# Performance work log

Measured on AMD Instinct MI355X. Metric: run time of the kernel, lower is better.

## Reference

```python
import jax, jax.numpy as jnp
import numpy as np

N_QUBITS = 12
N_LAYERS = 4
INPUT_DIM = 64
N_CLASSES = 4
BATCH = 2048


def _ry_mat(theta):
    # RY(t) = [[cos t/2, -sin t/2], [sin t/2, cos t/2]], returned as [..., 2, 2] complex64
    c = jnp.cos(theta / 2).astype(jnp.complex64)
    s = jnp.sin(theta / 2).astype(jnp.complex64)
    return jnp.stack([jnp.stack([c, -s], -1), jnp.stack([s, c], -1)], -2)


def _rz_mat(theta):
    # RZ(t) = diag(e^{-i t/2}, e^{+i t/2}), [..., 2, 2] complex64
    ph = jnp.exp((-0.5j) * theta).astype(jnp.complex64)
    z = jnp.zeros_like(ph)
    return jnp.stack([jnp.stack([ph, z], -1), jnp.stack([z, jnp.conj(ph)], -1)], -2)


def _apply_1q_batched(state, gate, wire):
    # state: [B] + [2]*n, gate: [B, 2, 2] (per-sample gate, e.g. angle encoding)
    ax = wire + 1
    st = jnp.moveaxis(state, ax, -1)
    st = jnp.einsum('b...i,bji->b...j', st, gate)
    return jnp.moveaxis(st, -1, ax)


def _apply_1q_shared(state, gate, wire):
    # state: [B] + [2]*n, gate: [2, 2] (shared trainable gate)
    ax = wire + 1
    st = jnp.moveaxis(state, ax, -1)
    st = jnp.einsum('...i,ji->...j', st, gate)
    return jnp.moveaxis(st, -1, ax)


def _cnot(state, control, target):
    ca, ta = control + 1, target + 1
    s0 = jax.lax.index_in_dim(state, 0, ca, keepdims=True)
    s1 = jax.lax.index_in_dim(state, 1, ca, keepdims=True)
    s1 = jnp.flip(s1, ta)  # X on target when control = 1
    return jnp.concatenate([s0, s1], axis=ca)


def _simulate(angles, qw):
    # angles: [B, n] encoding angles; qw: [L, n, 2] variational params
    B, n = angles.shape
    state = jnp.zeros((B,) + (2,) * n, jnp.complex64)
    state = state.at[(slice(None),) + (0,) * n].set(1.0 + 0.0j)
    enc = _ry_mat(angles)  # [B, n, 2, 2]
    for q in range(n):
        state = _apply_1q_batched(state, enc[:, q], q)
    for l in range(qw.shape[0]):
        ryg = _ry_mat(qw[l, :, 0])  # [n, 2, 2]
        rzg = _rz_mat(qw[l, :, 1])  # [n, 2, 2]
        for q in range(n):
            state = _apply_1q_shared(state, ryg[q], q)
            state = _apply_1q_shared(state, rzg[q], q)
        for q in range(n - 1):
            state = _cnot(state, q, q + 1)
        if n > 1:
            state = _cnot(state, n - 1, 0)
    p = state.real ** 2 + state.imag ** 2  # probabilities, [B] + [2]*n
    zs = []
    for q in range(n):
        m = jnp.moveaxis(p, q + 1, 1).reshape(B, 2, -1).sum(-1)  # [B, 2]
        zs.append(m[:, 0] - m[:, 1])
    return jnp.stack(zs, -1)  # [B, n] PauliZ expectations


def setup_inputs() -> dict:
    key = jax.random.key(0)
    ks = jax.random.split(key, 4)
    x = jax.random.normal(ks[0], (BATCH, INPUT_DIM), dtype=jnp.float32)
    W_in = 0.1 * jax.random.normal(ks[1], (N_QUBITS, INPUT_DIM), dtype=jnp.float32)
    b_in = jnp.zeros((N_QUBITS,), dtype=jnp.float32)
    qw = 0.01 * jax.random.normal(ks[2], (N_LAYERS, N_QUBITS, 2), dtype=jnp.float32)
    W_out = 0.1 * jax.random.normal(ks[3], (N_CLASSES, N_QUBITS), dtype=jnp.float32)
    b_out = jnp.zeros((N_CLASSES,), dtype=jnp.float32)
    return {"compressed_features": x, "W_in": W_in, "b_in": b_in, "qw": qw,
            "W_out": W_out, "b_out": b_out}


def reference(compressed_features, W_in, b_in, qw, W_out, b_out):
    angles = jnp.tanh(compressed_features @ W_in.T + b_in) * jnp.float32(np.pi)  # [B, n]
    zfeat = _simulate(angles, qw)  # [B, n]
    return zfeat @ W_out.T + b_out  # [B, n_classes]
```

## Files before the change

### kernel.cpp

```cpp
#include <hip/hip_runtime.h>
#include <math.h>

#define NQ    12
#define NST   4096
#define NL    4
#define NBATCH 2048
#define DIM   64
#define NCLS  4
#define TPB   512
#define APT   8

typedef float v2f __attribute__((ext_vector_type(2)));

constexpr unsigned Pm(unsigned j) { return j ^ (j >> 1) ^ ((j & 1u) * 0xC00u); }

constexpr unsigned Lm(unsigned j) {
    return (j & ~0x1Fu) | ((j ^ (j >> 3)) & 0xFu) | ((((j >> 4) ^ (j >> 8)) & 1u) << 4);
}

__device__ __forceinline__ unsigned beta_of(int lane, int wv) {
    return ((unsigned)(lane >> 4) & 1u)       | (((unsigned)wv & 1u) << 1)
         | (((unsigned)(wv >> 1) & 1u) << 2)  | (((unsigned)(wv >> 2) & 1u) << 3)
         | (((unsigned)(lane >> 2) & 1u) << 4)| (((unsigned)lane & 1u) << 5)
         | (((unsigned)(lane >> 5) & 1u) << 6)| (((unsigned)(lane >> 1) & 1u) << 7)
         | (((unsigned)(lane >> 3) & 1u) << 8);
}

__device__ __forceinline__ v2f cmul(v2f x, v2f y) {
    v2f r; r.x = x.x*y.x - x.y*y.y; r.y = x.x*y.y + x.y*y.x; return r;
}

template<int XB>
__device__ __forceinline__ float lx(float v) {
    int i = __float_as_int(v);
    if constexpr (XB == 1) {
        return __int_as_float(__builtin_amdgcn_update_dpp(i, i, 0xB1, 0xF, 0xF, true));
    } else if constexpr (XB == 2) {
        return __int_as_float(__builtin_amdgcn_update_dpp(i, i, 0x4E, 0xF, 0xF, true));
    } else {
        return __int_as_float(__builtin_amdgcn_update_dpp(i, i, 0x128, 0xF, 0xF, true));
    }
}

template<int P>
__device__ __forceinline__ void intra_g(v2f (&a)[APT], float c, float s) {
    #pragma unroll
    for (int k = 0; k < APT; ++k) {
        if (!(k & (1 << P))) {
            const int k1 = k | (1 << P);
            v2f x0 = a[k], x1 = a[k1];
            a[k]  = c*x0 - s*x1;
            a[k1] = s*x0 + c*x1;
        }
    }
}

template<int XB>
__device__ __forceinline__ void lane_g(v2f (&a)[APT], float c, float s, int lane) {
    const float Br = (lane & XB) ? s : -s;
    #pragma unroll
    for (int k = 0; k < APT; ++k) {
        v2f o; o.x = lx<XB>(a[k].x); o.y = lx<XB>(a[k].y);
        a[k] = c*a[k] + Br*o;
    }
}

__device__ __forceinline__ void gates_A(v2f (&a)[APT], const float* __restrict__ cs, int lane) {
    intra_g<0>(a, cs[11*2], cs[11*2+1]);
    intra_g<1>(a, cs[10*2], cs[10*2+1]);
    intra_g<2>(a, cs[ 9*2], cs[ 9*2+1]);
    lane_g<1>(a, cs[8*2], cs[8*2+1], lane);
    lane_g<2>(a, cs[7*2], cs[7*2+1], lane);
    lane_g<8>(a, cs[5*2], cs[5*2+1], lane);
}
__device__ __forceinline__ void gates_B(v2f (&a)[APT], const float* __restrict__ cs, int lane) {
    intra_g<0>(a, cs[2*2], cs[2*2+1]);
    intra_g<1>(a, cs[1*2], cs[1*2+1]);
    intra_g<2>(a, cs[0*2], cs[0*2+1]);
    lane_g<1>(a, cs[6*2], cs[6*2+1], lane);
    lane_g<2>(a, cs[4*2], cs[4*2+1], lane);
    lane_g<8>(a, cs[3*2], cs[3*2+1], lane);
}

__global__ void vqc_setup(const float* __restrict__ qw, float* __restrict__ gp) {
    const int t = threadIdx.x;
    const int lane = t & 63, wv = t >> 6;
    if (t < 36) {
        int l = t / 12 + 1, q = t % 12;
        float th = qw[(l*NQ + q)*2];
        float cc, ss; sincosf(0.5f*th, &ss, &cc);
        gp[((l-1)*NQ + q)*2 + 0] = cc;
        gp[((l-1)*NQ + q)*2 + 1] = ss;
    }
    if (t >= 64 && t < 80) {
        int i = t - 64, l = i/8 + 1, k = i%8;
        float ang = 0.f;
        if (k & 1) ang += qw[(l*NQ + 2)*2 + 1];
        if (k & 2) ang += qw[(l*NQ + 1)*2 + 1];
        if (k & 4) ang += qw[(l*NQ + 0)*2 + 1];
        float s_, c_; sincosf(ang, &s_, &c_);
        gp[72 + (l-1)*16 + k*2 + 0] = c_;
        gp[72 + (l-1)*16 + k*2 + 1] = s_;
    }
    const unsigned be = beta_of(lane, wv);
    #pragma unroll
    for (int l = 1; l <= 2; ++l) {
        float ang = 0.f;
        #pragma unroll
        for (int b = 0; b <= 8; ++b)
            if ((be >> b) & 1) ang += qw[(l*NQ + (11 - b))*2 + 1];
        float s_, c_; sincosf(ang, &s_, &c_);
        gp[104 + (l-1)*1024 + t*2 + 0] = c_;
        gp[104 + (l-1)*1024 + t*2 + 1] = s_;
    }
}

__global__ __launch_bounds__(TPB, 4) void vqc_kernel(
    const float* __restrict__ x,
    const float* __restrict__ Win,
    const float* __restrict__ bin,
    const float* __restrict__ qw,
    const float* __restrict__ Wout,
    const float* __restrict__ bout,
    const float* __restrict__ gp,
    float* __restrict__ out)
{
    __shared__ __align__(16) v2f buf[NST];
    __shared__ float xs[DIM];
    __shared__ float g0c[NQ], g0r[NQ], g0i[NQ];
    __shared__ float zred[8][9];
    __shared__ float zfin[NQ];

    const int tid  = threadIdx.x;
    const int lane = tid & 63;
    const int wv   = tid >> 6;
    const int b    = blockIdx.x;

    const unsigned al  = (unsigned)tid << 3;
    const unsigned be  = beta_of(lane, wv);
    const unsigned LA1 = Lm(al),      LB1 = Lm(be);
    const unsigned LA2 = Lm(Pm(al)),  LB2 = Lm(Pm(be));
    const unsigned LA3 = Lm(Pm(Pm(al))), LB3 = Lm(Pm(Pm(be)));

    if (tid < DIM) xs[tid] = x[b*DIM + tid];
    __syncthreads();

    if (tid < 192) {
        const int q = tid >> 4, r = tid & 15;
        float acc = xs[r] * Win[q*DIM + r]
                  + xs[r+16] * Win[q*DIM + r + 16]
                  + xs[r+32] * Win[q*DIM + r + 32]
                  + xs[r+48] * Win[q*DIM + r + 48];
        acc += __shfl_xor(acc, 8, 16);
        acc += __shfl_xor(acc, 4, 16);
        acc += __shfl_xor(acc, 2, 16);
        acc += __shfl_xor(acc, 1, 16);
        if (r == 0) {
            acc += bin[q];
            float ang = tanhf(acc) * 3.14159265358979323846f;
            float th  = ang + qw[(0*NQ + q)*2 + 0];
            float ph  = qw[(0*NQ + q)*2 + 1];
            float cc, ss; sincosf(0.5f*th, &ss, &cc);
            float pcv, psv; sincosf(ph, &psv, &pcv);
            g0c[q] = cc; g0r[q] = ss*pcv; g0i[q] = ss*psv;
        }
    }
    __syncthreads();

    v2f a[APT];

    {
        const unsigned nb = Pm(al);
        v2f thrP = (v2f){1.f, 0.f};
        #pragma unroll
        for (int bb = 3; bb <= 9; ++bb) {
            const int q = 11 - bb;
            const bool bit = (nb >> bb) & 1u;
            v2f f; f.x = bit ? g0r[q] : g0c[q]; f.y = bit ? g0i[q] : 0.f;
            thrP = cmul(thrP, f);
        }
        const bool n10 = (nb >> 10) & 1u, n11 = (nb >> 11) & 1u;
        v2f f1b; f1b.x = n10 ? g0r[1] : g0c[1]; f1b.y = n10 ? g0i[1] : 0.f;
        v2f f1x; f1x.x = n10 ? g0c[1] : g0r[1]; f1x.y = n10 ? 0.f : g0i[1];
        v2f f0b; f0b.x = n11 ? g0r[0] : g0c[0]; f0b.y = n11 ? g0i[0] : 0.f;
        v2f f0x; f0x.x = n11 ? g0c[0] : g0r[0]; f0x.y = n11 ? 0.f : g0i[0];
        v2f C0 = cmul(thrP, cmul(f1b, f0b));
        v2f C1 = cmul(thrP, cmul(f1x, f0x));
        const bool n0 = nb & 1u, n1 = (nb >> 1) & 1u, n2 = (nb >> 2) & 1u;
        v2f fa; fa.x = n0 ? g0r[11] : g0c[11]; fa.y = n0 ? g0i[11] : 0.f;
        v2f fb; fb.x = n0 ? g0c[11] : g0r[11]; fb.y = n0 ? 0.f : g0i[11];
        v2f E0 = cmul(C0, fa), E1 = cmul(C0, fb);
        v2f F0 = cmul(C1, fb), F1 = cmul(C1, fa);
        v2f u10; u10.x = n1 ? g0r[10] : g0c[10]; u10.y = n1 ? g0i[10] : 0.f;
        v2f w10; w10.x = n1 ? g0c[10] : g0r[10]; w10.y = n1 ? 0.f : g0i[10];
        v2f u9;  u9.x  = n2 ? g0r[9]  : g0c[9];  u9.y  = n2 ? g0i[9]  : 0.f;
        v2f w9;  w9.x  = n2 ? g0c[9]  : g0r[9];  w9.y  = n2 ? 0.f : g0i[9];
        v2f G0 = cmul(u10, u9), G1 = cmul(w10, u9), G2 = cmul(w10, w9), G3 = cmul(u10, w9);
        a[0] = cmul(E0, G0); a[1] = cmul(F0, G0);
        a[2] = cmul(E1, G1); a[3] = cmul(F1, G1);
        a[4] = cmul(E0, G2); a[5] = cmul(F0, G2);
        a[6] = cmul(E1, G3); a[7] = cmul(F1, G3);
    }

    const float* cs1 = gp;
    const float* cs2 = gp + 24;
    const float* cs3 = gp + 48;
    const v2f thrD1 = *(const v2f*)(gp + 104 + tid*2);
    const v2f thrD2 = *(const v2f*)(gp + 104 + 1024 + tid*2);

    gates_A(a, cs1, lane);
    {
        float4* f4 = (float4*)buf;
        const bool a0 = LA1 & 1u;
        #pragma unroll
        for (int ke = 0; ke < APT; ke += 2) {
            v2f lo = a0 ? a[ke+1] : a[ke];
            v2f hi = a0 ? a[ke]   : a[ke+1];
            f4[(LA1 ^ (unsigned)ke) >> 1] = make_float4(lo.x, lo.y, hi.x, hi.y);
        }
    }
    __syncthreads();
    #pragma unroll
    for (int k = 0; k < APT; ++k) a[k] = buf[LB1 ^ ((unsigned)k << 9)];
    gates_B(a, cs1, lane);
    #pragma unroll
    for (int k = 0; k < APT; ++k) {
        v2f kd = *(const v2f*)(gp + 72 + k*2);
        a[k] = cmul(a[k], cmul(thrD1, kd));
    }
    #pragma unroll
    for (int k = 0; k < APT; ++k) buf[LB1 ^ ((unsigned)k << 9)] = a[k];
    __syncthreads();

    #pragma unroll
    for (int k = 0; k < APT; ++k) a[k] = buf[LA2 ^ Lm(Pm((unsigned)k))];
    gates_A(a, cs2, lane);
    #pragma unroll
    for (int k = 0; k < APT; ++k) buf[LA2 ^ Lm(Pm((unsigned)k))] = a[k];
    __syncthreads();
    #pragma unroll
    for (int k = 0; k < APT; ++k) a[k] = buf[LB2 ^ Lm(Pm((unsigned)k << 9))];
    gates_B(a, cs2, lane);
    #pragma unroll
    for (int k = 0; k < APT; ++k) {
        v2f kd = *(const v2f*)(gp + 72 + 16 + k*2);
        a[k] = cmul(a[k], cmul(thrD2, kd));
    }
    #pragma unroll
    for (int k = 0; k < APT; ++k) buf[LB2 ^ Lm(Pm((unsigned)k << 9))] = a[k];
    __syncthreads();

    #pragma unroll
    for (int k = 0; k < APT; ++k) a[k] = buf[LA3 ^ Lm(Pm(Pm((unsigned)k)))];
    gates_A(a, cs3, lane);
    #pragma unroll
    for (int k = 0; k < APT; ++k) buf[LA3 ^ Lm(Pm(Pm((unsigned)k)))] = a[k];
    __syncthreads();
    #pragma unroll
    for (int k = 0; k < APT; ++k) a[k] = buf[LB3 ^ Lm(Pm(Pm((unsigned)k << 9)))];
    gates_B(a, cs3, lane);

    {
        float p[APT];
        #pragma unroll
        for (int k = 0; k < APT; ++k) p[k] = a[k].x*a[k].x + a[k].y*a[k].y;
        float A = (p[0]-p[1]) - (p[2]-p[3]), B = (p[4]-p[5]) - (p[6]-p[7]);
        float C = (p[0]+p[1]) - (p[2]+p[3]), D = (p[4]+p[5]) - (p[6]+p[7]);
        float w7 = A - B;
        float w3 = A + B;
        float w6 = C - D;
        #pragma unroll
        for (int t = 0; t < 6; ++t) {
            float o7 = __shfl_xor(w7, 1 << t, 64);
            float o6 = __shfl_xor(w6, 1 << t, 64);
            float o3 = __shfl_xor(w3, 1 << t, 64);
            const bool hi = (lane >> t) & 1;
            w7 = hi ? (o7 - w7) : (w7 + o7);
            w6 = hi ? (o6 - w6) : (w6 + o6);
            w3 = hi ? (o3 - w3) : (w3 + o3);
        }
        if      (lane == 63) { zred[wv][0] = w7; zred[wv][8] = w3; }
        else if (lane == 47) { zred[wv][1] = w7; }
        else if (lane == 43) { zred[wv][2] = w7; }
        else if (lane == 42) { zred[wv][3] = w7; }
        else if (lane == 10) { zred[wv][4] = w7; }
        else if (lane ==  8) { zred[wv][5] = w7; }
        else if (lane ==  0) { zred[wv][6] = w7; zred[wv][7] = w6; }
    }
    __syncthreads();
    if (tid < NQ) {
        const int p = 11 - tid;
        const int slot = (p == 0) ? 0 : (p <= 4) ? 1 : (p - 3);
        const int wm = (p <= 1 || p == 11) ? 7 : (p == 2) ? 6 : (p == 3) ? 4 : 0;
        float acc = 0.f;
        #pragma unroll
        for (int W = 0; W < 8; ++W) {
            float v = zred[W][slot];
            acc += (__popc(W & wm) & 1) ? -v : v;
        }
        zfin[tid] = acc;
    }
    __syncthreads();

    if (tid < NCLS) {
        float acc = bout[tid];
        #pragma unroll
        for (int q = 0; q < NQ; ++q) acc += zfin[q] * Wout[tid*NQ + q];
        out[b*NCLS + tid] = acc;
    }
}

extern "C" void kernel_launch(void* const* d_in, const int* in_sizes, int n_in,
                              void* d_out, int out_size, void* d_ws, size_t ws_size,
                              hipStream_t stream) {
    const float* x    = (const float*)d_in[0];
    const float* Win  = (const float*)d_in[1];
    const float* bin  = (const float*)d_in[2];
    const float* qw   = (const float*)d_in[3];
    const float* Wout = (const float*)d_in[4];
    const float* bout = (const float*)d_in[5];
    float* gp  = (float*)d_ws;
    float* out = (float*)d_out;
    hipLaunchKernelGGL(vqc_setup, dim3(1), dim3(TPB), 0, stream, qw, gp);
    hipLaunchKernelGGL(vqc_kernel, dim3(NBATCH), dim3(TPB), 0, stream,
                       x, Win, bin, qw, Wout, bout, gp, out);
}
```

Baseline: 53.37 us.

## Halve threads per block with 16 amplitudes per thread and new swizzle

Each block now uses 256 threads, and each thread holds 16 state amplitudes instead of 8. Four qubits are applied in registers per pass, with two via DPP lane exchanges, so the 8-way xor lane gate is dropped. The shared-memory swizzle, the phase tables and the final Z-reduction bit bookkeeping are all rewritten for this layout. Gate math uses packed v_pk_fma/v_pk_mul instructions, and the separate store loop after the diagonal phase is fused into the multiply. This removes one DPP gate type and halves wave count per block, but it raises register pressure and reduces parallelism per block.

```diff
diff --git a/kernel.cpp b/kernel.cpp
--- a/kernel.cpp
+++ b/kernel.cpp
@@ -3,115 +3,113 @@
 
 #define NQ    12
 #define NST   4096
-#define NL    4
 #define NBATCH 2048
 #define DIM   64
 #define NCLS  4
-#define TPB   512
-#define APT   8
+#define TPB   256
+#define APT   16
 
 typedef float v2f __attribute__((ext_vector_type(2)));
 
 constexpr unsigned Pm(unsigned j) { return j ^ (j >> 1) ^ ((j & 1u) * 0xC00u); }
-
-constexpr unsigned Lm(unsigned j) {
-    return (j & ~0x1Fu) | ((j ^ (j >> 3)) & 0xFu) | ((((j >> 4) ^ (j >> 8)) & 1u) << 4);
-}
-
-__device__ __forceinline__ unsigned beta_of(int lane, int wv) {
-    return ((unsigned)(lane >> 4) & 1u)       | (((unsigned)wv & 1u) << 1)
-         | (((unsigned)(wv >> 1) & 1u) << 2)  | (((unsigned)(wv >> 2) & 1u) << 3)
-         | (((unsigned)(lane >> 2) & 1u) << 4)| (((unsigned)lane & 1u) << 5)
-         | (((unsigned)(lane >> 5) & 1u) << 6)| (((unsigned)(lane >> 1) & 1u) << 7)
-         | (((unsigned)(lane >> 3) & 1u) << 8);
+constexpr unsigned Sm(unsigned j) { return j ^ ((j >> 4) & 0xFu); }
+
+__device__ __forceinline__ unsigned alphaA(unsigned t) { return t << 4; }
+__device__ __forceinline__ unsigned alphaB(unsigned t) {
+    unsigned lane = t & 63u, w = t >> 6;
+    return ((lane >> 2) & 0xFu) | (w << 4) | ((lane & 3u) << 6);
 }
 
 __device__ __forceinline__ v2f cmul(v2f x, v2f y) {
     v2f r; r.x = x.x*y.x - x.y*y.y; r.y = x.x*y.y + x.y*y.x; return r;
+}
+
+__device__ __forceinline__ v2f pk_mul(v2f a, v2f b) {
+    v2f d; asm("v_pk_mul_f32 %0, %1, %2" : "=v"(d) : "v"(a), "v"(b)); return d;
+}
+__device__ __forceinline__ v2f pk_fma(v2f a, v2f b, v2f c) {
+    v2f d; asm("v_pk_fma_f32 %0, %1, %2, %3" : "=v"(d) : "v"(a), "v"(b), "v"(c)); return d;
 }
 
 template<int XB>
 __device__ __forceinline__ float lx(float v) {
     int i = __float_as_int(v);
-    if constexpr (XB == 1) {
+    if constexpr (XB == 1)
         return __int_as_float(__builtin_amdgcn_update_dpp(i, i, 0xB1, 0xF, 0xF, true));
-    } else if constexpr (XB == 2) {
+    else
         return __int_as_float(__builtin_amdgcn_update_dpp(i, i, 0x4E, 0xF, 0xF, true));
-    } else {
-        return __int_as_float(__builtin_amdgcn_update_dpp(i, i, 0x128, 0xF, 0xF, true));
-    }
 }
 
 template<int P>
 __device__ __forceinline__ void intra_g(v2f (&a)[APT], float c, float s) {
+    const v2f cc = {c, c}, ss = {s, s}, ns = {-s, -s};
     #pragma unroll
     for (int k = 0; k < APT; ++k) {
         if (!(k & (1 << P))) {
             const int k1 = k | (1 << P);
             v2f x0 = a[k], x1 = a[k1];
-            a[k]  = c*x0 - s*x1;
-            a[k1] = s*x0 + c*x1;
+            a[k]  = pk_fma(ns, x1, pk_mul(cc, x0));
+            a[k1] = pk_fma(cc, x1, pk_mul(ss, x0));
         }
     }
 }
 
 template<int XB>
 __device__ __forceinline__ void lane_g(v2f (&a)[APT], float c, float s, int lane) {
-    const float Br = (lane & XB) ? s : -s;
+    const float br = (lane & XB) ? s : -s;
+    const v2f cc = {c, c}, bb = {br, br};
     #pragma unroll
     for (int k = 0; k < APT; ++k) {
         v2f o; o.x = lx<XB>(a[k].x); o.y = lx<XB>(a[k].y);
-        a[k] = c*a[k] + Br*o;
+        a[k] = pk_fma(bb, o, pk_mul(cc, a[k]));
     }
 }
 
 __device__ __forceinline__ void gates_A(v2f (&a)[APT], const float* __restrict__ cs, int lane) {
-    intra_g<0>(a, cs[11*2], cs[11*2+1]);
-    intra_g<1>(a, cs[10*2], cs[10*2+1]);
-    intra_g<2>(a, cs[ 9*2], cs[ 9*2+1]);
-    lane_g<1>(a, cs[8*2], cs[8*2+1], lane);
-    lane_g<2>(a, cs[7*2], cs[7*2+1], lane);
-    lane_g<8>(a, cs[5*2], cs[5*2+1], lane);
+    intra_g<0>(a, cs[22], cs[23]);
+    intra_g<1>(a, cs[20], cs[21]);
+    intra_g<2>(a, cs[18], cs[19]);
+    intra_g<3>(a, cs[16], cs[17]);
+    lane_g<1>(a, cs[14], cs[15], lane);
+    lane_g<2>(a, cs[12], cs[13], lane);
 }
 __device__ __forceinline__ void gates_B(v2f (&a)[APT], const float* __restrict__ cs, int lane) {
-    intra_g<0>(a, cs[2*2], cs[2*2+1]);
-    intra_g<1>(a, cs[1*2], cs[1*2+1]);
-    intra_g<2>(a, cs[0*2], cs[0*2+1]);
-    lane_g<1>(a, cs[6*2], cs[6*2+1], lane);
-    lane_g<2>(a, cs[4*2], cs[4*2+1], lane);
-    lane_g<8>(a, cs[3*2], cs[3*2+1], lane);
+    intra_g<0>(a, cs[6], cs[7]);
+    intra_g<1>(a, cs[4], cs[5]);
+    intra_g<2>(a, cs[2], cs[3]);
+    intra_g<3>(a, cs[0], cs[1]);
+    lane_g<1>(a, cs[10], cs[11], lane);
+    lane_g<2>(a, cs[8],  cs[9],  lane);
 }
 
 __global__ void vqc_setup(const float* __restrict__ qw, float* __restrict__ gp) {
     const int t = threadIdx.x;
-    const int lane = t & 63, wv = t >> 6;
     if (t < 36) {
         int l = t / 12 + 1, q = t % 12;
-        float th = qw[(l*NQ + q)*2];
-        float cc, ss; sincosf(0.5f*th, &ss, &cc);
-        gp[((l-1)*NQ + q)*2 + 0] = cc;
-        gp[((l-1)*NQ + q)*2 + 1] = ss;
-    }
-    if (t >= 64 && t < 80) {
-        int i = t - 64, l = i/8 + 1, k = i%8;
+        float cc, ss; sincosf(0.5f * qw[(l*NQ + q)*2], &ss, &cc);
+        gp[(l-1)*24 + q*2 + 0] = cc;
+        gp[(l-1)*24 + q*2 + 1] = ss;
+    }
+    if (t < 32) {
+        int l = t / 16 + 1, k = t % 16;
         float ang = 0.f;
-        if (k & 1) ang += qw[(l*NQ + 2)*2 + 1];
-        if (k & 2) ang += qw[(l*NQ + 1)*2 + 1];
-        if (k & 4) ang += qw[(l*NQ + 0)*2 + 1];
+        #pragma unroll
+        for (int i = 0; i < 4; ++i)
+            if ((k >> i) & 1) ang += qw[(l*NQ + (3 - i))*2 + 1];
         float s_, c_; sincosf(ang, &s_, &c_);
-        gp[72 + (l-1)*16 + k*2 + 0] = c_;
-        gp[72 + (l-1)*16 + k*2 + 1] = s_;
-    }
-    const unsigned be = beta_of(lane, wv);
+        gp[72 + (l-1)*32 + k*2 + 0] = c_;
+        gp[72 + (l-1)*32 + k*2 + 1] = s_;
+    }
+    const unsigned j = alphaB((unsigned)t);
     #pragma unroll
     for (int l = 1; l <= 2; ++l) {
         float ang = 0.f;
         #pragma unroll
-        for (int b = 0; b <= 8; ++b)
-            if ((be >> b) & 1) ang += qw[(l*NQ + (11 - b))*2 + 1];
+        for (int b = 0; b < 8; ++b)
+            if ((j >> b) & 1) ang += qw[(l*NQ + (11 - b))*2 + 1];
         float s_, c_; sincosf(ang, &s_, &c_);
-        gp[104 + (l-1)*1024 + t*2 + 0] = c_;
-        gp[104 + (l-1)*1024 + t*2 + 1] = s_;
+        gp[136 + (l-1)*512 + t*2 + 0] = c_;
+        gp[136 + (l-1)*512 + t*2 + 1] = s_;
     }
 }
 
@@ -128,7 +126,7 @@
     __shared__ __align__(16) v2f buf[NST];
     __shared__ float xs[DIM];
     __shared__ float g0c[NQ], g0r[NQ], g0i[NQ];
-    __shared__ float zred[8][9];
+    __shared__ float zred[4][10];
     __shared__ float zfin[NQ];
 
     const int tid  = threadIdx.x;
@@ -136,11 +134,10 @@
     const int wv   = tid >> 6;
     const int b    = blockIdx.x;
 
-    const unsigned al  = (unsigned)tid << 3;
-    const unsigned be  = beta_of(lane, wv);
-    const unsigned LA1 = Lm(al),      LB1 = Lm(be);
-    const unsigned LA2 = Lm(Pm(al)),  LB2 = Lm(Pm(be));
-    const unsigned LA3 = Lm(Pm(Pm(al))), LB3 = Lm(Pm(Pm(be)));
+    const unsigned aA = alphaA((unsigned)tid), aB = alphaB((unsigned)tid);
+    const unsigned A1 = Sm(aA),         B1 = Sm(aB);
+    const unsigned A2 = Sm(Pm(aA)),     B2 = Sm(Pm(aB));
+    const unsigned A3 = Sm(Pm(Pm(aA))), B3 = Sm(Pm(Pm(aB)));
 
     if (tid < DIM) xs[tid] = x[b*DIM + tid];
     __syncthreads();
@@ -170,132 +167,143 @@
     v2f a[APT];
 
     {
-        const unsigned nb = Pm(al);
+        const unsigned nb = Pm(aA);
         v2f thrP = (v2f){1.f, 0.f};
         #pragma unroll
-        for (int bb = 3; bb <= 9; ++bb) {
+        for (int bb = 4; bb <= 9; ++bb) {
             const int q = 11 - bb;
             const bool bit = (nb >> bb) & 1u;
             v2f f; f.x = bit ? g0r[q] : g0c[q]; f.y = bit ? g0i[q] : 0.f;
             thrP = cmul(thrP, f);
         }
         const bool n10 = (nb >> 10) & 1u, n11 = (nb >> 11) & 1u;
-        v2f f1b; f1b.x = n10 ? g0r[1] : g0c[1]; f1b.y = n10 ? g0i[1] : 0.f;
-        v2f f1x; f1x.x = n10 ? g0c[1] : g0r[1]; f1x.y = n10 ? 0.f : g0i[1];
-        v2f f0b; f0b.x = n11 ? g0r[0] : g0c[0]; f0b.y = n11 ? g0i[0] : 0.f;
-        v2f f0x; f0x.x = n11 ? g0c[0] : g0r[0]; f0x.y = n11 ? 0.f : g0i[0];
-        v2f C0 = cmul(thrP, cmul(f1b, f0b));
-        v2f C1 = cmul(thrP, cmul(f1x, f0x));
-        const bool n0 = nb & 1u, n1 = (nb >> 1) & 1u, n2 = (nb >> 2) & 1u;
-        v2f fa; fa.x = n0 ? g0r[11] : g0c[11]; fa.y = n0 ? g0i[11] : 0.f;
-        v2f fb; fb.x = n0 ? g0c[11] : g0r[11]; fb.y = n0 ? 0.f : g0i[11];
-        v2f E0 = cmul(C0, fa), E1 = cmul(C0, fb);
-        v2f F0 = cmul(C1, fb), F1 = cmul(C1, fa);
-        v2f u10; u10.x = n1 ? g0r[10] : g0c[10]; u10.y = n1 ? g0i[10] : 0.f;
-        v2f w10; w10.x = n1 ? g0c[10] : g0r[10]; w10.y = n1 ? 0.f : g0i[10];
-        v2f u9;  u9.x  = n2 ? g0r[9]  : g0c[9];  u9.y  = n2 ? g0i[9]  : 0.f;
-        v2f w9;  w9.x  = n2 ? g0c[9]  : g0r[9];  w9.y  = n2 ? 0.f : g0i[9];
-        v2f G0 = cmul(u10, u9), G1 = cmul(w10, u9), G2 = cmul(w10, w9), G3 = cmul(u10, w9);
-        a[0] = cmul(E0, G0); a[1] = cmul(F0, G0);
-        a[2] = cmul(E1, G1); a[3] = cmul(F1, G1);
-        a[4] = cmul(E0, G2); a[5] = cmul(F0, G2);
-        a[6] = cmul(E1, G3); a[7] = cmul(F1, G3);
-    }
-
-    const float* cs1 = gp;
-    const float* cs2 = gp + 24;
-    const float* cs3 = gp + 48;
-    const v2f thrD1 = *(const v2f*)(gp + 104 + tid*2);
-    const v2f thrD2 = *(const v2f*)(gp + 104 + 1024 + tid*2);
+        v2f h10a; h10a.x = n10 ? g0r[1] : g0c[1]; h10a.y = n10 ? g0i[1] : 0.f;
+        v2f h10b; h10b.x = n10 ? g0c[1] : g0r[1]; h10b.y = n10 ? 0.f : g0i[1];
+        v2f h11a; h11a.x = n11 ? g0r[0] : g0c[0]; h11a.y = n11 ? g0i[0] : 0.f;
+        v2f h11b; h11b.x = n11 ? g0c[0] : g0r[0]; h11b.y = n11 ? 0.f : g0i[0];
+        v2f TT0 = cmul(thrP, cmul(h10a, h11a));
+        v2f TT1 = cmul(thrP, cmul(h10b, h11b));
+        v2f u[4], w[4];
+        #pragma unroll
+        for (int bb = 0; bb < 4; ++bb) {
+            const int q = 11 - bb;
+            const bool bit = (nb >> bb) & 1u;
+            u[bb].x = bit ? g0r[q] : g0c[q]; u[bb].y = bit ? g0i[q] : 0.f;
+            w[bb].x = bit ? g0c[q] : g0r[q]; w[bb].y = bit ? 0.f : g0i[q];
+        }
+        v2f P01[4], P23[4];
+        #pragma unroll
+        for (int c = 0; c < 4; ++c) {
+            P01[c] = cmul((c & 1) ? w[0] : u[0], (c & 2) ? w[1] : u[1]);
+            P23[c] = cmul((c & 1) ? w[2] : u[2], (c & 2) ? w[3] : u[3]);
+        }
+        #pragma unroll
+        for (int k = 0; k < APT; ++k) {
+            const unsigned kp = (unsigned)k ^ ((unsigned)k >> 1);
+            v2f g = cmul(P01[kp & 3], P23[(kp >> 2) & 3]);
+            a[k] = cmul((k & 1) ? TT1 : TT0, g);
+        }
+    }
+
+    const float* cs1 = gp, *cs2 = gp + 24, *cs3 = gp + 48;
+    const v2f tD1 = *(const v2f*)(gp + 136 + tid*2);
+    const v2f tD2 = *(const v2f*)(gp + 136 + 512 + tid*2);
 
     gates_A(a, cs1, lane);
     {
         float4* f4 = (float4*)buf;
-        const bool a0 = LA1 & 1u;
+        const int a0 = (int)(A1 & 1u);
         #pragma unroll
         for (int ke = 0; ke < APT; ke += 2) {
             v2f lo = a0 ? a[ke+1] : a[ke];
             v2f hi = a0 ? a[ke]   : a[ke+1];
-            f4[(LA1 ^ (unsigned)ke) >> 1] = make_float4(lo.x, lo.y, hi.x, hi.y);
-        }
-    }
-    __syncthreads();
-    #pragma unroll
-    for (int k = 0; k < APT; ++k) a[k] = buf[LB1 ^ ((unsigned)k << 9)];
+            f4[(A1 ^ (unsigned)ke) >> 1] = make_float4(lo.x, lo.y, hi.x, hi.y);
+        }
+    }
+    __syncthreads();
+    #pragma unroll
+    for (int k = 0; k < APT; ++k) a[k] = buf[B1 ^ ((unsigned)k << 8)];
     gates_B(a, cs1, lane);
     #pragma unroll
     for (int k = 0; k < APT; ++k) {
         v2f kd = *(const v2f*)(gp + 72 + k*2);
-        a[k] = cmul(a[k], cmul(thrD1, kd));
-    }
-    #pragma unroll
-    for (int k = 0; k < APT; ++k) buf[LB1 ^ ((unsigned)k << 9)] = a[k];
-    __syncthreads();
-
-    #pragma unroll
-    for (int k = 0; k < APT; ++k) a[k] = buf[LA2 ^ Lm(Pm((unsigned)k))];
+        buf[B1 ^ ((unsigned)k << 8)] = cmul(cmul(a[k], tD1), kd);
+    }
+    __syncthreads();
+
+    #pragma unroll
+    for (int k = 0; k < APT; ++k) a[k] = buf[A2 ^ Sm(Pm((unsigned)k))];
     gates_A(a, cs2, lane);
     #pragma unroll
-    for (int k = 0; k < APT; ++k) buf[LA2 ^ Lm(Pm((unsigned)k))] = a[k];
-    __syncthreads();
-    #pragma unroll
-    for (int k = 0; k < APT; ++k) a[k] = buf[LB2 ^ Lm(Pm((unsigned)k << 9))];
+    for (int k = 0; k < APT; ++k) buf[A2 ^ Sm(Pm((unsigned)k))] = a[k];
+    __syncthreads();
+    #pragma unroll
+    for (int k = 0; k < APT; ++k) a[k] = buf[B2 ^ Sm(Pm((unsigned)k << 8))];
     gates_B(a, cs2, lane);
     #pragma unroll
     for (int k = 0; k < APT; ++k) {
-        v2f kd = *(const v2f*)(gp + 72 + 16 + k*2);
-        a[k] = cmul(a[k], cmul(thrD2, kd));
-    }
-    #pragma unroll
-    for (int k = 0; k < APT; ++k) buf[LB2 ^ Lm(Pm((unsigned)k << 9))] = a[k];
-    __syncthreads();
-
-    #pragma unroll
-    for (int k = 0; k < APT; ++k) a[k] = buf[LA3 ^ Lm(Pm(Pm((unsigned)k)))];
+        v2f kd = *(const v2f*)(gp + 72 + 32 + k*2);
+        buf[B2 ^ Sm(Pm((unsigned)k << 8))] = cmul(cmul(a[k], tD2), kd);
+    }
+    __syncthreads();
+
+    #pragma unroll
+    for (int k = 0; k < APT; ++k) a[k] = buf[A3 ^ Sm(Pm(Pm((unsigned)k)))];
     gates_A(a, cs3, lane);
     #pragma unroll
-    for (int k = 0; k < APT; ++k) buf[LA3 ^ Lm(Pm(Pm((unsigned)k)))] = a[k];
-    __syncthreads();
-    #pragma unroll
-    for (int k = 0; k < APT; ++k) a[k] = buf[LB3 ^ Lm(Pm(Pm((unsigned)k << 9)))];
+    for (int k = 0; k < APT; ++k) buf[A3 ^ Sm(Pm(Pm((unsigned)k)))] = a[k];
+    __syncthreads();
+    #pragma unroll
+    for (int k = 0; k < APT; ++k) a[k] = buf[B3 ^ Sm(Pm(Pm((unsigned)k << 8)))];
     gates_B(a, cs3, lane);
 
     {
         float p[APT];
         #pragma unroll
-        for (int k = 0; k < APT; ++k) p[k] = a[k].x*a[k].x + a[k].y*a[k].y;
-        float A = (p[0]-p[1]) - (p[2]-p[3]), B = (p[4]-p[5]) - (p[6]-p[7]);
-        float C = (p[0]+p[1]) - (p[2]+p[3]), D = (p[4]+p[5]) - (p[6]+p[7]);
-        float w7 = A - B;
-        float w3 = A + B;
-        float w6 = C - D;
+        for (int k = 0; k < APT; ++k) p[k] = fmaf(a[k].x, a[k].x, a[k].y*a[k].y);
+        float A_[8], Bm[8];
+        #pragma unroll
+        for (int j = 0; j < 8; ++j) { A_[j] = p[2*j] + p[2*j+1]; Bm[j] = p[2*j] - p[2*j+1]; }
+        float AA[4], AB[4], BB[4];
+        #pragma unroll
+        for (int i = 0; i < 4; ++i) {
+            AA[i] = A_[2*i] + A_[2*i+1];
+            AB[i] = A_[2*i] - A_[2*i+1];
+            BB[i] = Bm[2*i] - Bm[2*i+1];
+        }
+        float WF = BB[0] - BB[1] - BB[2] + BB[3];
+        float W7 = BB[0] - BB[1] + BB[2] - BB[3];
+        float WE = AB[0] - AB[1] - AB[2] + AB[3];
+        float WC = AA[0] - AA[1] - AA[2] + AA[3];
         #pragma unroll
         for (int t = 0; t < 6; ++t) {
-            float o7 = __shfl_xor(w7, 1 << t, 64);
-            float o6 = __shfl_xor(w6, 1 << t, 64);
-            float o3 = __shfl_xor(w3, 1 << t, 64);
+            float oF = __shfl_xor(WF, 1 << t, 64);
+            float o7 = __shfl_xor(W7, 1 << t, 64);
+            float oE = __shfl_xor(WE, 1 << t, 64);
+            float oC = __shfl_xor(WC, 1 << t, 64);
             const bool hi = (lane >> t) & 1;
-            w7 = hi ? (o7 - w7) : (w7 + o7);
-            w6 = hi ? (o6 - w6) : (w6 + o6);
-            w3 = hi ? (o3 - w3) : (w3 + o3);
-        }
-        if      (lane == 63) { zred[wv][0] = w7; zred[wv][8] = w3; }
-        else if (lane == 47) { zred[wv][1] = w7; }
-        else if (lane == 43) { zred[wv][2] = w7; }
-        else if (lane == 42) { zred[wv][3] = w7; }
-        else if (lane == 10) { zred[wv][4] = w7; }
-        else if (lane ==  8) { zred[wv][5] = w7; }
-        else if (lane ==  0) { zred[wv][6] = w7; zred[wv][7] = w6; }
+            WF = hi ? (oF - WF) : (WF + oF);
+            W7 = hi ? (o7 - W7) : (W7 + o7);
+            WE = hi ? (oE - WE) : (WE + oE);
+            WC = hi ? (oC - WC) : (WC + oC);
+        }
+        if      (lane == 63) { zred[wv][0] = WF; zred[wv][9] = W7; }
+        else if (lane == 59) { zred[wv][1] = WF; }
+        else if (lane == 51) { zred[wv][2] = WF; }
+        else if (lane == 35) { zred[wv][3] = WF; }
+        else if (lane ==  3) { zred[wv][4] = WF; }
+        else if (lane ==  2) { zred[wv][5] = WF; }
+        else if (lane ==  0) { zred[wv][6] = WF; zred[wv][7] = WE; zred[wv][8] = WC; }
     }
     __syncthreads();
     if (tid < NQ) {
-        const int p = 11 - tid;
-        const int slot = (p == 0) ? 0 : (p <= 4) ? 1 : (p - 3);
-        const int wm = (p <= 1 || p == 11) ? 7 : (p == 2) ? 6 : (p == 3) ? 4 : 0;
+        const int slotT[12] = {9,8,7,6,5,4,4,4,3,2,1,0};
+        const int wmT[12]   = {3,0,0,0,0,0,2,3,3,3,3,3};
+        const int sl = slotT[tid], wm = wmT[tid];
         float acc = 0.f;
         #pragma unroll
-        for (int W = 0; W < 8; ++W) {
-            float v = zred[W][slot];
+        for (int W = 0; W < 4; ++W) {
+            float v = zred[W][sl];
             acc += (__popc(W & wm) & 1) ? -v : v;
         }
         zfin[tid] = acc;
```

Measured after the change: 51.45 us. -3.6%, faster.

## Swap LDS swizzles for per-phase XOR maps and use packed FMA gates

Applied to the files above, without the earlier changes.

Replaces the single Lm shared-memory swizzle with separate per-phase XOR maps (T1m/T2m/T4m), so the read and write addresses of a phase can differ. This needs an extra barrier before each write-back. The single-qubit rotations now use inline-asm v_pk_mul/v_pk_fma on complex pairs to halve VALU instruction count. Launch bounds rise to 8 waves per EU, which may increase register pressure or spilling. The aim is fewer LDS bank conflicts and fewer ALU ops, at the cost of extra synchronisation.

```diff
diff --git a/kernel.cpp b/kernel.cpp
--- a/kernel.cpp
+++ b/kernel.cpp
@@ -3,7 +3,6 @@
 
 #define NQ    12
 #define NST   4096
-#define NL    4
 #define NBATCH 2048
 #define DIM   64
 #define NCLS  4
@@ -13,12 +12,18 @@
 typedef float v2f __attribute__((ext_vector_type(2)));
 
 constexpr unsigned Pm(unsigned j) { return j ^ (j >> 1) ^ ((j & 1u) * 0xC00u); }
-
-constexpr unsigned Lm(unsigned j) {
-    return (j & ~0x1Fu) | ((j ^ (j >> 3)) & 0xFu) | ((((j >> 4) ^ (j >> 8)) & 1u) << 4);
-}
-
-__device__ __forceinline__ unsigned beta_of(int lane, int wv) {
+constexpr unsigned Pm2(unsigned j) { return Pm(Pm(j)); }
+
+constexpr unsigned T1m(unsigned j) { return j ^ ((j >> 5) & 0xFu); }
+constexpr unsigned T2m(unsigned j) {
+    return T1m(j) ^ ((((j >> 6) ^ (j >> 8)) & 1u) << 4);
+}
+constexpr unsigned T4m(unsigned j) {
+    return j ^ ((j >> 8) & 1u) ^ (((j >> 7) & 1u) << 1) ^ (((j >> 6) & 1u) << 2)
+             ^ (((j >> 7) & 1u) << 3) ^ (((j >> 5) & 1u) << 4);
+}
+
+__device__ __host__ __forceinline__ unsigned beta_of(int lane, int wv) {
     return ((unsigned)(lane >> 4) & 1u)       | (((unsigned)wv & 1u) << 1)
          | (((unsigned)(wv >> 1) & 1u) << 2)  | (((unsigned)(wv >> 2) & 1u) << 3)
          | (((unsigned)(lane >> 2) & 1u) << 4)| (((unsigned)lane & 1u) << 5)
@@ -28,6 +33,13 @@
 
 __device__ __forceinline__ v2f cmul(v2f x, v2f y) {
     v2f r; r.x = x.x*y.x - x.y*y.y; r.y = x.x*y.y + x.y*y.x; return r;
+}
+
+__device__ __forceinline__ v2f pk_mul(v2f a, v2f b) {
+    v2f d; asm("v_pk_mul_f32 %0, %1, %2" : "=v"(d) : "v"(a), "v"(b)); return d;
+}
+__device__ __forceinline__ v2f pk_fma(v2f a, v2f b, v2f c) {
+    v2f d; asm("v_pk_fma_f32 %0, %1, %2, %3" : "=v"(d) : "v"(a), "v"(b), "v"(c)); return d;
 }
 
 template<int XB>
@@ -44,42 +56,44 @@
 
 template<int P>
 __device__ __forceinline__ void intra_g(v2f (&a)[APT], float c, float s) {
+    const v2f cc = {c, c}, ss = {s, s}, ns = {-s, -s};
     #pragma unroll
     for (int k = 0; k < APT; ++k) {
         if (!(k & (1 << P))) {
             const int k1 = k | (1 << P);
             v2f x0 = a[k], x1 = a[k1];
-            a[k]  = c*x0 - s*x1;
-            a[k1] = s*x0 + c*x1;
+            a[k]  = pk_fma(ns, x1, pk_mul(cc, x0));
+            a[k1] = pk_fma(cc, x1, pk_mul(ss, x0));
         }
     }
 }
 
 template<int XB>
 __device__ __forceinline__ void lane_g(v2f (&a)[APT], float c, float s, int lane) {
-    const float Br = (lane & XB) ? s : -s;
+    const float br = (lane & XB) ? s : -s;
+    const v2f cc = {c, c}, bb = {br, br};
     #pragma unroll
     for (int k = 0; k < APT; ++k) {
         v2f o; o.x = lx<XB>(a[k].x); o.y = lx<XB>(a[k].y);
-        a[k] = c*a[k] + Br*o;
+        a[k] = pk_fma(bb, o, pk_mul(cc, a[k]));
     }
 }
 
 __device__ __forceinline__ void gates_A(v2f (&a)[APT], const float* __restrict__ cs, int lane) {
-    intra_g<0>(a, cs[11*2], cs[11*2+1]);
-    intra_g<1>(a, cs[10*2], cs[10*2+1]);
-    intra_g<2>(a, cs[ 9*2], cs[ 9*2+1]);
-    lane_g<1>(a, cs[8*2], cs[8*2+1], lane);
-    lane_g<2>(a, cs[7*2], cs[7*2+1], lane);
-    lane_g<8>(a, cs[5*2], cs[5*2+1], lane);
+    intra_g<0>(a, cs[22], cs[23]);
+    intra_g<1>(a, cs[20], cs[21]);
+    intra_g<2>(a, cs[18], cs[19]);
+    lane_g<1>(a, cs[16], cs[17], lane);
+    lane_g<2>(a, cs[14], cs[15], lane);
+    lane_g<8>(a, cs[10], cs[11], lane);
 }
 __device__ __forceinline__ void gates_B(v2f (&a)[APT], const float* __restrict__ cs, int lane) {
-    intra_g<0>(a, cs[2*2], cs[2*2+1]);
-    intra_g<1>(a, cs[1*2], cs[1*2+1]);
-    intra_g<2>(a, cs[0*2], cs[0*2+1]);
-    lane_g<1>(a, cs[6*2], cs[6*2+1], lane);
-    lane_g<2>(a, cs[4*2], cs[4*2+1], lane);
-    lane_g<8>(a, cs[3*2], cs[3*2+1], lane);
+    intra_g<0>(a, cs[4],  cs[5]);
+    intra_g<1>(a, cs[2],  cs[3]);
+    intra_g<2>(a, cs[0],  cs[1]);
+    lane_g<1>(a, cs[12], cs[13], lane);
+    lane_g<2>(a, cs[8],  cs[9],  lane);
+    lane_g<8>(a, cs[6],  cs[7],  lane);
 }
 
 __global__ void vqc_setup(const float* __restrict__ qw, float* __restrict__ gp) {
@@ -115,7 +129,7 @@
     }
 }
 
-__global__ __launch_bounds__(TPB, 4) void vqc_kernel(
+__global__ __launch_bounds__(TPB, 8) void vqc_kernel(
     const float* __restrict__ x,
     const float* __restrict__ Win,
     const float* __restrict__ bin,
@@ -136,11 +150,16 @@
     const int wv   = tid >> 6;
     const int b    = blockIdx.x;
 
-    const unsigned al  = (unsigned)tid << 3;
-    const unsigned be  = beta_of(lane, wv);
-    const unsigned LA1 = Lm(al),      LB1 = Lm(be);
-    const unsigned LA2 = Lm(Pm(al)),  LB2 = Lm(Pm(be));
-    const unsigned LA3 = Lm(Pm(Pm(al))), LB3 = Lm(Pm(Pm(be)));
+    const unsigned aA = (unsigned)tid << 3;
+    const unsigned aB = beta_of(lane, wv);
+    const unsigned A1  = T1m(aA);
+    const unsigned B1r = T1m(aB);
+    const unsigned B1w = T2m(aB);
+    const unsigned A2  = T2m(Pm(aA));
+    const unsigned B2r = T2m(Pm(aB));
+    const unsigned B2w = T4m(Pm(aB));
+    const unsigned A3  = T4m(Pm2(aA));
+    const unsigned B3  = T4m(Pm2(aB));
 
     if (tid < DIM) xs[tid] = x[b*DIM + tid];
     __syncthreads();
@@ -170,7 +189,7 @@
     v2f a[APT];
 
     {
-        const unsigned nb = Pm(al);
+        const unsigned nb = Pm(aA);
         v2f thrP = (v2f){1.f, 0.f};
         #pragma unroll
         for (int bb = 3; bb <= 9; ++bb) {
@@ -205,65 +224,76 @@
     const float* cs1 = gp;
     const float* cs2 = gp + 24;
     const float* cs3 = gp + 48;
-    const v2f thrD1 = *(const v2f*)(gp + 104 + tid*2);
-    const v2f thrD2 = *(const v2f*)(gp + 104 + 1024 + tid*2);
+    const v2f tD1 = *(const v2f*)(gp + 104 + tid*2);
+    const v2f tD2 = *(const v2f*)(gp + 104 + 1024 + tid*2);
 
     gates_A(a, cs1, lane);
     {
         float4* f4 = (float4*)buf;
-        const bool a0 = LA1 & 1u;
+        const int a0 = (int)(A1 & 1u);
         #pragma unroll
         for (int ke = 0; ke < APT; ke += 2) {
             v2f lo = a0 ? a[ke+1] : a[ke];
             v2f hi = a0 ? a[ke]   : a[ke+1];
-            f4[(LA1 ^ (unsigned)ke) >> 1] = make_float4(lo.x, lo.y, hi.x, hi.y);
-        }
-    }
-    __syncthreads();
-    #pragma unroll
-    for (int k = 0; k < APT; ++k) a[k] = buf[LB1 ^ ((unsigned)k << 9)];
+            f4[(A1 ^ (unsigned)ke) >> 1] = make_float4(lo.x, lo.y, hi.x, hi.y);
+        }
+    }
+    __syncthreads();
+    #pragma unroll
+    for (int k = 0; k < APT; ++k)
+        a[k] = buf[B1r ^ ((unsigned)k << 9)];
     gates_B(a, cs1, lane);
     #pragma unroll
     for (int k = 0; k < APT; ++k) {
         v2f kd = *(const v2f*)(gp + 72 + k*2);
-        a[k] = cmul(a[k], cmul(thrD1, kd));
-    }
-    #pragma unroll
-    for (int k = 0; k < APT; ++k) buf[LB1 ^ ((unsigned)k << 9)] = a[k];
-    __syncthreads();
-
-    #pragma unroll
-    for (int k = 0; k < APT; ++k) a[k] = buf[LA2 ^ Lm(Pm((unsigned)k))];
+        a[k] = cmul(cmul(a[k], tD1), kd);
+    }
+    __syncthreads();
+    #pragma unroll
+    for (int k = 0; k < APT; ++k)
+        buf[B1w ^ ((unsigned)k << 9)] = a[k];
+    __syncthreads();
+
+    #pragma unroll
+    for (int k = 0; k < APT; ++k)
+        a[k] = buf[A2 ^ T2m(Pm((unsigned)k))];
     gates_A(a, cs2, lane);
     #pragma unroll
-    for (int k = 0; k < APT; ++k) buf[LA2 ^ Lm(Pm((unsigned)k))] = a[k];
-    __syncthreads();
-    #pragma unroll
-    for (int k = 0; k < APT; ++k) a[k] = buf[LB2 ^ Lm(Pm((unsigned)k << 9))];
+    for (int k = 0; k < APT; ++k)
+        buf[A2 ^ T2m(Pm((unsigned)k))] = a[k];
+    __syncthreads();
+    #pragma unroll
+    for (int k = 0; k < APT; ++k)
+        a[k] = buf[B2r ^ T2m(Pm((unsigned)k << 9))];
     gates_B(a, cs2, lane);
     #pragma unroll
     for (int k = 0; k < APT; ++k) {
         v2f kd = *(const v2f*)(gp + 72 + 16 + k*2);
-        a[k] = cmul(a[k], cmul(thrD2, kd));
-    }
-    #pragma unroll
-    for (int k = 0; k < APT; ++k) buf[LB2 ^ Lm(Pm((unsigned)k << 9))] = a[k];
-    __syncthreads();
-
-    #pragma unroll
-    for (int k = 0; k < APT; ++k) a[k] = buf[LA3 ^ Lm(Pm(Pm((unsigned)k)))];
+        a[k] = cmul(cmul(a[k], tD2), kd);
+    }
+    __syncthreads();
+    #pragma unroll
+    for (int k = 0; k < APT; ++k)
+        buf[B2w ^ T4m(Pm((unsigned)k << 9))] = a[k];
+    __syncthreads();
+
+    #pragma unroll
+    for (int k = 0; k < APT; ++k)
+        a[k] = buf[A3 ^ T4m(Pm2((unsigned)k))];
     gates_A(a, cs3, lane);
     #pragma unroll
-    for (int k = 0; k < APT; ++k) buf[LA3 ^ Lm(Pm(Pm((unsigned)k)))] = a[k];
-    __syncthreads();
-    #pragma unroll
-    for (int k = 0; k < APT; ++k) a[k] = buf[LB3 ^ Lm(Pm(Pm((unsigned)k << 9)))];
+    for (int k = 0; k < APT; ++k)
+        buf[A3 ^ T4m(Pm2((unsigned)k))] = a[k];
+    __syncthreads();
+    #pragma unroll
+    for (int k = 0; k < APT; ++k)
+        a[k] = buf[B3 ^ T4m(Pm2((unsigned)k << 9))];
     gates_B(a, cs3, lane);
 
     {
         float p[APT];
         #pragma unroll
-        for (int k = 0; k < APT; ++k) p[k] = a[k].x*a[k].x + a[k].y*a[k].y;
+        for (int k = 0; k < APT; ++k) p[k] = fmaf(a[k].x, a[k].x, a[k].y*a[k].y);
         float A = (p[0]-p[1]) - (p[2]-p[3]), B = (p[4]-p[5]) - (p[6]-p[7]);
         float C = (p[0]+p[1]) - (p[2]+p[3]), D = (p[4]+p[5]) - (p[6]+p[7]);
         float w7 = A - B;
```

New measurement: 56.36 us. 5.6% more time.
